# Performance work log

Hardware: AMD Instinct MI355X
Metric: run time of the kernel (lower is better)

The kernel has to match this reference:

```python
import jax, jax.numpy as jnp
import numpy as np

K = 3  # TAGConv default number of hops
N, E = 50000, 800000
F_X, F_POS, HID, OUT = 6, 2, 64, 10


def _tagconv(x, W, b, src, dst, norm, n):
    # TAGConv: out = sum_{k=0}^{K} (A_norm^k x) @ W[k] + b
    out = x @ W[0]
    h = x
    for k in range(1, K + 1):
        # one propagate step: gather from src, weight, scatter-sum to dst
        h = jax.ops.segment_sum(norm[:, None] * h[src], dst, num_segments=n)
        out = out + h @ W[k]
    return out + b


def setup_inputs() -> dict:
    key = jax.random.key(0)
    ks = jax.random.split(key, 12)
    x = jax.random.normal(ks[0], (N, F_X), dtype=jnp.float32)
    pos = jax.random.normal(ks[1], (N, F_POS), dtype=jnp.float32)
    edge_index = jax.random.randint(ks[2], (2, E), 0, N, dtype=jnp.int64)
    edge_attr = jax.random.uniform(ks[3], (E,), dtype=jnp.float32)
    s = 0.1
    W1 = jax.random.normal(ks[4], (K + 1, F_X + F_POS, HID), dtype=jnp.float32) * s
    b1 = jnp.zeros((HID,), dtype=jnp.float32)
    W2 = jax.random.normal(ks[5], (K + 1, HID, HID), dtype=jnp.float32) * s
    b2 = jnp.zeros((HID,), dtype=jnp.float32)
    W3 = jax.random.normal(ks[6], (K + 1, HID, OUT), dtype=jnp.float32) * s
    b3 = jnp.zeros((OUT,), dtype=jnp.float32)
    return {"x": x, "pos": pos, "edge_attr": edge_attr,
            "W1": W1, "b1": b1, "W2": W2, "b2": b2, "W3": W3, "b3": b3,
            "edge_index": edge_index}


def reference(x, pos, edge_attr, W1, b1, W2, b2, W3, b3, edge_index):
    n = x.shape[0]
    src, dst = edge_index[0], edge_index[1]
    # gcn_norm (no self loops, as in TAGConv): deg over destination (col)
    deg = jax.ops.segment_sum(edge_attr, dst, num_segments=n)
    dinv = jnp.where(deg > 0, jax.lax.rsqrt(deg), jnp.zeros_like(deg))
    norm = dinv[src] * edge_attr * dinv[dst]
    h = jnp.concatenate([x, pos], axis=1)
    h = jax.nn.relu(_tagconv(h, W1, b1, src, dst, norm, n))
    # F.dropout with training=False is identity (eval reference)
    h = jax.nn.relu(_tagconv(h, W2, b2, src, dst, norm, n))
    h = _tagconv(h, W3, b3, src, dst, norm, n)
    return jax.nn.log_softmax(h, axis=1)
```

## Files before the change

kernel.cpp:

```cpp
#include <hip/hip_runtime.h>
#include <math.h>


#define NN 50000
#define EE 800000
#define HID 64
#define NOUT 10
#define CH 512

#define NB 391
#define CAP 2400
#define K1_EPB 4096

typedef __attribute__((ext_vector_type(8))) short bf16x8;
typedef __attribute__((ext_vector_type(4))) float f32x4;

__device__ __forceinline__ unsigned bf16rnd(float x) {
    unsigned u = __float_as_uint(x);
    return (u + 0x7FFFu + ((u >> 16) & 1u)) >> 16;
}
__device__ __forceinline__ unsigned packbf2(float a, float b) {
    return bf16rnd(a) | (bf16rnd(b) << 16);
}
__device__ __forceinline__ float bflo(unsigned u) { return __uint_as_float(u << 16); }
__device__ __forceinline__ float bfhi(unsigned u) { return __uint_as_float(u & 0xFFFF0000u); }

__global__ __launch_bounds__(512) void bucket_scatter_kernel(
        const int* __restrict__ src, const int* __restrict__ dst,
        const float* __restrict__ ea, int* __restrict__ cursor,
        int2* __restrict__ regions, int e) {
    __shared__ int hist[NB];
    __shared__ int base[NB];
    int tid = threadIdx.x;
    int e0 = blockIdx.x * K1_EPB;
    int e1 = e0 + K1_EPB; if (e1 > e) e1 = e;
    for (int i = tid; i < NB; i += 512) hist[i] = 0;
    __syncthreads();
    for (int i = e0 + tid; i < e1; i += 512)
        atomicAdd(&hist[dst[i] >> 7], 1);
    __syncthreads();
    for (int b = tid; b < NB; b += 512) {
        int c = hist[b];
        base[b] = (c > 0) ? atomicAdd(&cursor[b], c) : 0;
        hist[b] = 0;
    }
    __syncthreads();
    for (int i = e0 + tid; i < e1; i += 512) {
        int d = dst[i];
        int b = d >> 7;
        int r = atomicAdd(&hist[b], 1);
        int pos = base[b] + r;
        if (pos < CAP)
            regions[(size_t)b * CAP + pos] =
                make_int2(((d & 127) << 16) | src[i], __float_as_int(ea[i]));
    }
}

__global__ __launch_bounds__(512) void bucket_build_kernel(
        const int* __restrict__ cursor, int2* __restrict__ regions,
        float* __restrict__ dinv, int* __restrict__ row_start, int n) {
    __shared__ int2 rec[CAP];
    __shared__ int hist[128];
    __shared__ float easum[128];
    __shared__ float dl[128];
    __shared__ int off[129];
    __shared__ int lcur[128];
    int b = blockIdx.x;
    int tid = threadIdx.x;
    int cnt = cursor[b]; if (cnt > CAP) cnt = CAP;
    size_t rb = (size_t)b * CAP;
    if (tid < 128) { hist[tid] = 0; easum[tid] = 0.f; lcur[tid] = 0; }
    __syncthreads();
    for (int i = tid; i < cnt; i += 512) {
        int2 r = regions[rb + i];
        rec[i] = r;
        int f = r.x >> 16;
        atomicAdd(&hist[f], 1);
        atomicAdd(&easum[f], __int_as_float(r.y));
    }
    __syncthreads();
    if (tid < 128) {
        int lane = tid & 63;
        int v = hist[tid];
        for (int o2 = 1; o2 < 64; o2 <<= 1) {
            int y = __shfl_up(v, o2, 64);
            if (lane >= o2) v += y;
        }
        off[tid + 1] = v;
        float s2 = easum[tid];
        dl[tid] = (s2 > 0.f) ? rsqrtf(s2) : 0.f;
    }
    __syncthreads();
    if (tid == 255) off[0] = 0;
    if (tid >= 64 && tid < 128) off[tid + 1] += off[64];
    __syncthreads();
    if (tid < 128) {
        int node = b * 128 + tid;
        if (node <= n) row_start[node] = b * CAP + off[tid];
        if (node < n)  dinv[node] = dl[tid];
    }
    __syncthreads();
    for (int i = tid; i < cnt; i += 512) {
        int2 r = rec[i];
        int f = r.x >> 16;
        int s = r.x & 0xFFFF;
        int p = atomicAdd(&lcur[f], 1);
        float w0 = __int_as_float(r.y) * dl[f];
        regions[rb + off[f] + p] = make_int2(s, __float_as_int(w0));
    }
}

__global__ __launch_bounds__(256) void srcscale_kernel(
        const int* __restrict__ cursor, const float* __restrict__ dinv,
        int2* __restrict__ regions) {
    int i = blockIdx.x * blockDim.x + threadIdx.x;
    int b = i / CAP;
    if (b >= NB) return;
    int off = i - b * CAP;
    int cnt = cursor[b]; if (cnt > CAP) cnt = CAP;
    if (off >= cnt) return;
    int2 r = regions[i];
    r.y = __float_as_int(__int_as_float(r.y) * dinv[r.x]);
    regions[i] = r;
}

__global__ __launch_bounds__(256) void pack1_kernel(const float* __restrict__ x,
                                                    const float* __restrict__ pos,
                                                    unsigned short* __restrict__ B1, int n) {
    int i = blockIdx.x * blockDim.x + threadIdx.x;
    if (i >= n) return;
    float2 a = *reinterpret_cast<const float2*>(x + (size_t)i * 6);
    float2 b = *reinterpret_cast<const float2*>(x + (size_t)i * 6 + 2);
    float2 c = *reinterpret_cast<const float2*>(x + (size_t)i * 6 + 4);
    float2 p = *reinterpret_cast<const float2*>(pos + (size_t)i * 2);
    uint4 o;
    o.x = packbf2(a.x, a.y);
    o.y = packbf2(b.x, b.y);
    o.z = packbf2(c.x, c.y);
    o.w = packbf2(p.x, p.y);
    *reinterpret_cast<uint4*>(B1 + (size_t)i * 32) = o;
}

__global__ __launch_bounds__(256) void prop8b_kernel(const int* __restrict__ row_start,
                                                     const int* __restrict__ cursor,
                                                     const int2* __restrict__ edges,
                                                     const unsigned short* __restrict__ Gin,
                                                     unsigned short* __restrict__ Gout, int n) {
    constexpr int TEAM = 8, NPB = 32;
    __shared__ int2 se[CH];
    int tid = threadIdx.x;
    int nb = blockIdx.x * NPB;
    int node = nb + tid / TEAM;
    int es = tid % TEAM;
    int nbEnd = (nb + NPB < n) ? (nb + NPB) : n;
    int bkt = nb >> 7;
    int cc = cursor[bkt]; if (cc > CAP) cc = CAP;
    int ce = bkt * CAP + cc;
    int blkBeg = row_start[nb];
    int blkEnd = row_start[nbEnd]; if (blkEnd > ce) blkEnd = ce;
    int beg = 0, end = 0;
    if (node < n) {
        beg = row_start[node];
        end = row_start[node + 1]; if (end > ce) end = ce;
    }
    float a0 = 0.f, a1 = 0.f, a2 = 0.f, a3 = 0.f, a4 = 0.f, a5 = 0.f, a6 = 0.f, a7 = 0.f;
    for (int base = blkBeg; base < blkEnd; base += CH) {
        int m = blkEnd - base; if (m > CH) m = CH;
        __syncthreads();
        for (int i = tid; i < m; i += 256) se[i] = edges[base + i];
        __syncthreads();
        int lo = (beg > base) ? (beg - base) : 0;
        int hi = ((end < base + m) ? end : (base + m)) - base;
        for (int i = lo + es; i < hi; i += TEAM) {
            int2 e = se[i];
            float w = __int_as_float(e.y);
            const uint4 v = *reinterpret_cast<const uint4*>(Gin + (size_t)e.x * 32);
            a0 += w * bflo(v.x); a1 += w * bfhi(v.x);
            a2 += w * bflo(v.y); a3 += w * bfhi(v.y);
            a4 += w * bflo(v.z); a5 += w * bfhi(v.z);
            a6 += w * bflo(v.w); a7 += w * bfhi(v.w);
        }
    }
    #pragma unroll
    for (int msk = 1; msk < TEAM; msk <<= 1) {
        a0 += __shfl_xor(a0, msk); a1 += __shfl_xor(a1, msk);
        a2 += __shfl_xor(a2, msk); a3 += __shfl_xor(a3, msk);
        a4 += __shfl_xor(a4, msk); a5 += __shfl_xor(a5, msk);
        a6 += __shfl_xor(a6, msk); a7 += __shfl_xor(a7, msk);
    }
    if (node < n && es == 0) {
        uint4 o;
        o.x = packbf2(a0, a1);
        o.y = packbf2(a2, a3);
        o.z = packbf2(a4, a5);
        o.w = packbf2(a6, a7);
        *reinterpret_cast<uint4*>(Gout + (size_t)node * 32) = o;
    }
}

template <int TPN, int ES, bool ACC>
__global__ __launch_bounds__(256) void prop_kernel(const int* __restrict__ row_start,
                                                   const int* __restrict__ cursor,
                                                   const int2* __restrict__ edges,
                                                   const float* __restrict__ hin, int in_stride,
                                                   float* __restrict__ hout, int out_stride, int n) {
    constexpr int TEAM = TPN * ES;
    constexpr int NPB = 256 / TEAM;
    __shared__ int2 se[CH];
    int tid = threadIdx.x;
    int nb = blockIdx.x * NPB;
    int node = nb + tid / TEAM;
    int t = tid % TEAM;
    int es = t / TPN;
    int lane = t % TPN;
    int nbEnd = (nb + NPB < n) ? (nb + NPB) : n;
    int bkt = nb >> 7;
    int cc = cursor[bkt]; if (cc > CAP) cc = CAP;
    int ce = bkt * CAP + cc;
    int blkBeg = row_start[nb];
    int blkEnd = row_start[nbEnd]; if (blkEnd > ce) blkEnd = ce;
    int beg = 0, end = 0;
    if (node < n) {
        beg = row_start[node];
        end = row_start[node + 1]; if (end > ce) end = ce;
    }
    float ax = 0.f, ay = 0.f, az = 0.f, aw = 0.f;
    for (int base = blkBeg; base < blkEnd; base += CH) {
        int m = blkEnd - base; if (m > CH) m = CH;
        __syncthreads();
        for (int i = tid; i < m; i += 256) se[i] = edges[base + i];
        __syncthreads();
        int lo = (beg > base) ? (beg - base) : 0;
        int hi = ((end < base + m) ? end : (base + m)) - base;
        for (int i = lo + es; i < hi; i += ES) {
            int2 e = se[i];
            float w = __int_as_float(e.y);
            const float4 v = *reinterpret_cast<const float4*>(hin + (size_t)e.x * in_stride + lane * 4);
            ax += w * v.x; ay += w * v.y; az += w * v.z; aw += w * v.w;
        }
    }
    #pragma unroll
    for (int msk = TPN; msk < TEAM; msk <<= 1) {
        ax += __shfl_xor(ax, msk);
        ay += __shfl_xor(ay, msk);
        az += __shfl_xor(az, msk);
        aw += __shfl_xor(aw, msk);
    }
    if (node < n && es == 0) {
        float4* po = reinterpret_cast<float4*>(hout + (size_t)node * out_stride + lane * 4);
        float4 r = make_float4(ax, ay, az, aw);
        if (ACC) { float4 o = *po; r.x += o.x; r.y += o.y; r.z += o.z; r.w += o.w; }
        *po = r;
    }
}

__global__ __launch_bounds__(256) void prop64b_kernel(const int* __restrict__ row_start,
                                                      const int* __restrict__ cursor,
                                                      const int2* __restrict__ edges,
                                                      const unsigned short* __restrict__ Gin,
                                                      unsigned short* __restrict__ Gout, int n) {
    constexpr int TPN = 8, ES = 4, TEAM = 32, NPB = 8;
    __shared__ int2 se[CH];
    int tid = threadIdx.x;
    int nb = blockIdx.x * NPB;
    int node = nb + tid / TEAM;
    int t = tid % TEAM;
    int es = t / TPN;
    int lane = t % TPN;
    int nbEnd = (nb + NPB < n) ? (nb + NPB) : n;
    int bkt = nb >> 7;
    int cc = cursor[bkt]; if (cc > CAP) cc = CAP;
    int ce = bkt * CAP + cc;
    int blkBeg = row_start[nb];
    int blkEnd = row_start[nbEnd]; if (blkEnd > ce) blkEnd = ce;
    int beg = 0, end = 0;
    if (node < n) {
        beg = row_start[node];
        end = row_start[node + 1]; if (end > ce) end = ce;
    }
    float a0 = 0.f, a1 = 0.f, a2 = 0.f, a3 = 0.f, a4 = 0.f, a5 = 0.f, a6 = 0.f, a7 = 0.f;
    for (int base = blkBeg; base < blkEnd; base += CH) {
        int m = blkEnd - base; if (m > CH) m = CH;
        __syncthreads();
        for (int i = tid; i < m; i += 256) se[i] = edges[base + i];
        __syncthreads();
        int lo = (beg > base) ? (beg - base) : 0;
        int hi = ((end < base + m) ? end : (base + m)) - base;
        for (int i = lo + es; i < hi; i += ES) {
            int2 e = se[i];
            float w = __int_as_float(e.y);
            const uint4 v = *reinterpret_cast<const uint4*>(Gin + (size_t)e.x * 256 + lane * 8);
            a0 += w * bflo(v.x); a1 += w * bfhi(v.x);
            a2 += w * bflo(v.y); a3 += w * bfhi(v.y);
            a4 += w * bflo(v.z); a5 += w * bfhi(v.z);
            a6 += w * bflo(v.w); a7 += w * bfhi(v.w);
        }
    }
    #pragma unroll
    for (int msk = TPN; msk < TEAM; msk <<= 1) {
        a0 += __shfl_xor(a0, msk); a1 += __shfl_xor(a1, msk);
        a2 += __shfl_xor(a2, msk); a3 += __shfl_xor(a3, msk);
        a4 += __shfl_xor(a4, msk); a5 += __shfl_xor(a5, msk);
        a6 += __shfl_xor(a6, msk); a7 += __shfl_xor(a7, msk);
    }
    if (node < n && es == 0) {
        uint4 o;
        o.x = packbf2(a0, a1);
        o.y = packbf2(a2, a3);
        o.z = packbf2(a4, a5);
        o.w = packbf2(a6, a7);
        *reinterpret_cast<uint4*>(Gout + (size_t)node * 256 + lane * 8) = o;
    }
}

__global__ __launch_bounds__(256) void prop_final_kernel(const int* __restrict__ row_start,
                                                         const int* __restrict__ cursor,
                                                         const int2* __restrict__ edges,
                                                         const float* __restrict__ hin,
                                                         const float* __restrict__ g0,
                                                         const float* __restrict__ b3,
                                                         float* __restrict__ out, int n) {
    constexpr int TPN = 4, ES = 2, TEAM = 8, NPB = 32;
    __shared__ int2 se[CH];
    int tid = threadIdx.x;
    int nb = blockIdx.x * NPB;
    int node = nb + tid / TEAM;
    int t = tid % TEAM;
    int es = t / TPN;
    int lane = t % TPN;
    int nbEnd = (nb + NPB < n) ? (nb + NPB) : n;
    int bkt = nb >> 7;
    int cc = cursor[bkt]; if (cc > CAP) cc = CAP;
    int ce = bkt * CAP + cc;
    int blkBeg = row_start[nb];
    int blkEnd = row_start[nbEnd]; if (blkEnd > ce) blkEnd = ce;
    int beg = 0, end = 0;
    if (node < n) {
        beg = row_start[node];
        end = row_start[node + 1]; if (end > ce) end = ce;
    }
    float ax = 0.f, ay = 0.f, az = 0.f, aw = 0.f;
    for (int base = blkBeg; base < blkEnd; base += CH) {
        int m = blkEnd - base; if (m > CH) m = CH;
        __syncthreads();
        for (int i = tid; i < m; i += 256) se[i] = edges[base + i];
        __syncthreads();
        int lo = (beg > base) ? (beg - base) : 0;
        int hi = ((end < base + m) ? end : (base + m)) - base;
        for (int i = lo + es; i < hi; i += ES) {
            int2 e = se[i];
            float w = __int_as_float(e.y);
            const float4 v = *reinterpret_cast<const float4*>(hin + (size_t)e.x * 64 + lane * 4);
            ax += w * v.x; ay += w * v.y; az += w * v.z; aw += w * v.w;
        }
    }
    ax += __shfl_xor(ax, TPN);
    ay += __shfl_xor(ay, TPN);
    az += __shfl_xor(az, TPN);
    aw += __shfl_xor(aw, TPN);
    if (node < n && es == 0) {
        const float4 g = *reinterpret_cast<const float4*>(g0 + (size_t)node * 64 + lane * 4);
        float vv[4] = {ax + g.x, ay + g.y, az + g.z, aw + g.w};
        int c0 = lane * 4;
        float mloc = -1e30f;
        #pragma unroll
        for (int c = 0; c < 4; ++c) {
            int col = c0 + c;
            if (col < NOUT) { vv[c] += b3[col]; mloc = fmaxf(mloc, vv[c]); }
        }
        float mo = fmaxf(mloc, __shfl_xor(mloc, 1));
        mo = fmaxf(mo, __shfl_xor(mo, 2));
        float sl = 0.f;
        #pragma unroll
        for (int c = 0; c < 4; ++c) {
            int col = c0 + c;
            if (col < NOUT) sl += __expf(vv[c] - mo);
        }
        sl += __shfl_xor(sl, 1);
        sl += __shfl_xor(sl, 2);
        float ls = __logf(sl);
        #pragma unroll
        for (int c = 0; c < 4; ++c) {
            int col = c0 + c;
            if (col < NOUT) out[(size_t)node * NOUT + col] = vv[c] - mo - ls;
        }
    }
}

template <int FIN, int KC, int EPI, int WMODE, int INBF16, int OUTBF16>
__global__ __launch_bounds__(256) void mm2_kernel(const void* __restrict__ hraw, int hstride,
                                                  const float* __restrict__ W,
                                                  const float* __restrict__ bias,
                                                  void* __restrict__ outraw, int ostride, int n) {
    constexpr int HP = 68;
    __shared__ float HsT[KC * HP];
    __shared__ float Ws[KC * 64];
    int tid = threadIdx.x;
    int ndq = tid >> 4;
    int f4  = tid & 15;
    int nd  = tid & 63;
    int wv  = tid >> 6;
    int nodeBase = blockIdx.x * 64;

    float4 acc0 = make_float4(0.f, 0.f, 0.f, 0.f);
    float4 acc1 = make_float4(0.f, 0.f, 0.f, 0.f);
    float4 acc2 = make_float4(0.f, 0.f, 0.f, 0.f);
    float4 acc3 = make_float4(0.f, 0.f, 0.f, 0.f);

    for (int kc = 0; kc < FIN; kc += KC) {
        if (WMODE == 0) {
            for (int i = tid * 4; i < KC * 64; i += 1024)
                *reinterpret_cast<float4*>(&Ws[i]) =
                    *reinterpret_cast<const float4*>(&W[(size_t)kc * 64 + i]);
        } else {
            for (int i = tid; i < KC * 64; i += 256) {
                int r = i >> 6, c = i & 63;
                int k = c >> 4, j = c & 15;
                Ws[i] = (j < NOUT) ? W[((size_t)k * FIN + kc + r) * NOUT + j] : 0.f;
            }
        }
        int node = nodeBase + nd;
        if constexpr (INBF16) {
            const unsigned short* hb = (const unsigned short*)hraw;
            constexpr int KPT = KC / 4;
            int k0 = wv * KPT;
            #pragma unroll
            for (int q = 0; q < KPT / 8; ++q) {
                uint4 v = make_uint4(0, 0, 0, 0);
                if (node < n)
                    v = *reinterpret_cast<const uint4*>(hb + (size_t)node * hstride + kc + k0 + q * 8);
                int kk = k0 + q * 8;
                HsT[(kk + 0) * HP + nd] = bflo(v.x); HsT[(kk + 1) * HP + nd] = bfhi(v.x);
                HsT[(kk + 2) * HP + nd] = bflo(v.y); HsT[(kk + 3) * HP + nd] = bfhi(v.y);
                HsT[(kk + 4) * HP + nd] = bflo(v.z); HsT[(kk + 5) * HP + nd] = bfhi(v.z);
                HsT[(kk + 6) * HP + nd] = bflo(v.w); HsT[(kk + 7) * HP + nd] = bfhi(v.w);
            }
        } else {
            const float* hf = (const float*)hraw;
            #pragma unroll
            for (int r = 0; r < KC / 16; ++r) {
                int k0 = wv * 4 + r * 16;
                float4 hv = make_float4(0.f, 0.f, 0.f, 0.f);
                if (node < n)
                    hv = *reinterpret_cast<const float4*>(&hf[(size_t)node * hstride + kc + k0]);
                HsT[(k0 + 0) * HP + nd] = hv.x;
                HsT[(k0 + 1) * HP + nd] = hv.y;
                HsT[(k0 + 2) * HP + nd] = hv.z;
                HsT[(k0 + 3) * HP + nd] = hv.w;
            }
        }
        __syncthreads();
        #pragma unroll 8
        for (int k = 0; k < KC; ++k) {
            const float4 hq = *reinterpret_cast<const float4*>(&HsT[k * HP + ndq * 4]);
            const float4 wq = *reinterpret_cast<const float4*>(&Ws[k * 64 + f4 * 4]);
            acc0.x += hq.x * wq.x; acc0.y += hq.x * wq.y; acc0.z += hq.x * wq.z; acc0.w += hq.x * wq.w;
            acc1.x += hq.y * wq.x; acc1.y += hq.y * wq.y; acc1.z += hq.y * wq.z; acc1.w += hq.y * wq.w;
            acc2.x += hq.z * wq.x; acc2.y += hq.z * wq.y; acc2.z += hq.z * wq.z; acc2.w += hq.z * wq.w;
            acc3.x += hq.w * wq.x; acc3.y += hq.w * wq.y; acc3.z += hq.w * wq.z; acc3.w += hq.w * wq.w;
        }
        __syncthreads();
    }

    float4 bv = make_float4(0.f, 0.f, 0.f, 0.f);
    if (EPI == 1) bv = *reinterpret_cast<const float4*>(&bias[f4 * 4]);
    float4 accs[4] = {acc0, acc1, acc2, acc3};
    #pragma unroll
    for (int i = 0; i < 4; ++i) {
        int node = nodeBase + ndq * 4 + i;
        if (node < n) {
            float4 a = accs[i];
            if (EPI == 1) {
                a.x = fmaxf(a.x + bv.x, 0.f); a.y = fmaxf(a.y + bv.y, 0.f);
                a.z = fmaxf(a.z + bv.z, 0.f); a.w = fmaxf(a.w + bv.w, 0.f);
            }
            if constexpr (OUTBF16) {
                unsigned short* ob = (unsigned short*)outraw;
                uint2 o;
                o.x = packbf2(a.x, a.y);
                o.y = packbf2(a.z, a.w);
                *reinterpret_cast<uint2*>(ob + (size_t)node * ostride + f4 * 4) = o;
            } else {
                float* of = (float*)outraw;
                *reinterpret_cast<float4*>(of + (size_t)node * ostride + f4 * 4) = a;
            }
        }
    }
}

__global__ __launch_bounds__(256) void mm23_kernel(const unsigned short* __restrict__ G,
                                                   const float* __restrict__ W2,
                                                   const float* __restrict__ b2,
                                                   const float* __restrict__ W3,
                                                   float* __restrict__ T, int n) {
    constexpr int HP = 68;
    __shared__ __align__(16) char smem[33792];
    unsigned short* w2s = (unsigned short*)smem;
    float* HsT = (float*)smem;
    float* Ws  = (float*)(smem + 64 * HP * 4);
    int tid = threadIdx.x;
    int wave = tid >> 6;
    int lane = tid & 63;
    int nodeBase = blockIdx.x * 64;

    for (int slot = tid; slot < 2048; slot += 256) {
        int l = slot & 63;
        int s = (slot >> 6) & 7;
        int t = slot >> 9;
        int k0 = s * 32 + ((l >> 4) << 3);
        int col = t * 16 + (l & 15);
        unsigned short tmp[8];
        #pragma unroll
        for (int j = 0; j < 8; ++j)
            tmp[j] = (unsigned short)bf16rnd(W2[(size_t)(k0 + j) * 64 + col]);
        *reinterpret_cast<uint4*>(w2s + slot * 8) = *reinterpret_cast<const uint4*>(tmp);
    }
    __syncthreads();

    int arow = nodeBase + wave * 16 + (lane & 15);
    bool aval = (arow < n);
    const unsigned short* arp = G + (size_t)arow * 256 + ((lane >> 4) << 3);
    f32x4 acc0 = {0.f, 0.f, 0.f, 0.f}, acc1 = {0.f, 0.f, 0.f, 0.f};
    f32x4 acc2 = {0.f, 0.f, 0.f, 0.f}, acc3 = {0.f, 0.f, 0.f, 0.f};
    #pragma unroll
    for (int s = 0; s < 8; ++s) {
        bf16x8 a = {};
        if (aval) a = *reinterpret_cast<const bf16x8*>(arp + s * 32);
        const unsigned short* wb = w2s + ((size_t)s * 64 + lane) * 8;
        bf16x8 bf0 = *reinterpret_cast<const bf16x8*>(wb);
        bf16x8 bf1 = *reinterpret_cast<const bf16x8*>(wb + 4096);
        bf16x8 bf2 = *reinterpret_cast<const bf16x8*>(wb + 8192);
        bf16x8 bf3 = *reinterpret_cast<const bf16x8*>(wb + 12288);
        acc0 = __builtin_amdgcn_mfma_f32_16x16x32_bf16(a, bf0, acc0, 0, 0, 0);
        acc1 = __builtin_amdgcn_mfma_f32_16x16x32_bf16(a, bf1, acc1, 0, 0, 0);
        acc2 = __builtin_amdgcn_mfma_f32_16x16x32_bf16(a, bf2, acc2, 0, 0, 0);
        acc3 = __builtin_amdgcn_mfma_f32_16x16x32_bf16(a, bf3, acc3, 0, 0, 0);
    }
    __syncthreads();

    {
        int c = lane & 15;
        int rbase = wave * 16 + (lane >> 4) * 4;
        f32x4 accs[4] = {acc0, acc1, acc2, acc3};
        #pragma unroll
        for (int t = 0; t < 4; ++t) {
            int col = t * 16 + c;
            float bb = b2[col];
            #pragma unroll
            for (int r = 0; r < 4; ++r) {
                float v = accs[t][r] + bb;
                HsT[col * HP + rbase + r] = v > 0.f ? v : 0.f;
            }
        }
    }
    for (int i = tid; i < 64 * 64; i += 256) {
        int r = i >> 6, c2 = i & 63;
        int k = c2 >> 4, j = c2 & 15;
        Ws[i] = (j < NOUT) ? W3[((size_t)k * 64 + r) * NOUT + j] : 0.f;
    }
    __syncthreads();

    int ndq = tid >> 4;
    int f4  = tid & 15;
    float4 t0 = make_float4(0.f, 0.f, 0.f, 0.f);
    float4 t1 = make_float4(0.f, 0.f, 0.f, 0.f);
    float4 t2 = make_float4(0.f, 0.f, 0.f, 0.f);
    float4 t3 = make_float4(0.f, 0.f, 0.f, 0.f);
    #pragma unroll 8
    for (int k = 0; k < 64; ++k) {
        const float4 hq = *reinterpret_cast<const float4*>(&HsT[k * HP + ndq * 4]);
        const float4 wq = *reinterpret_cast<const float4*>(&Ws[k * 64 + f4 * 4]);
        t0.x += hq.x * wq.x; t0.y += hq.x * wq.y; t0.z += hq.x * wq.z; t0.w += hq.x * wq.w;
        t1.x += hq.y * wq.x; t1.y += hq.y * wq.y; t1.z += hq.y * wq.z; t1.w += hq.y * wq.w;
        t2.x += hq.z * wq.x; t2.y += hq.z * wq.y; t2.z += hq.z * wq.z; t2.w += hq.z * wq.w;
        t3.x += hq.w * wq.x; t3.y += hq.w * wq.y; t3.z += hq.w * wq.z; t3.w += hq.w * wq.w;
    }
    float4 ts[4] = {t0, t1, t2, t3};
    #pragma unroll
    for (int i = 0; i < 4; ++i) {
        int node = nodeBase + ndq * 4 + i;
        if (node < n)
            *reinterpret_cast<float4*>(T + (size_t)node * 64 + f4 * 4) = ts[i];
    }
}

extern "C" void kernel_launch(void* const* d_in, const int* in_sizes, int n_in,
                              void* d_out, int out_size, void* d_ws, size_t ws_size,
                              hipStream_t stream) {
    const float* x   = (const float*)d_in[0];
    const float* pos = (const float*)d_in[1];
    const float* ea  = (const float*)d_in[2];
    const float* W1  = (const float*)d_in[3];
    const float* b1  = (const float*)d_in[4];
    const float* W2  = (const float*)d_in[5];
    const float* b2  = (const float*)d_in[6];
    const float* W3  = (const float*)d_in[7];
    const float* b3  = (const float*)d_in[8];
    const int* eidx  = (const int*)d_in[9];
    const int* src = eidx;
    const int* dst = eidx + EE;
    float* outp = (float*)d_out;

    size_t off = 0;
    char* base = (char*)d_ws;
    auto alloc = [&](size_t bytes) -> void* {
        void* p = base + off;
        off += (bytes + 255) & ~(size_t)255;
        return p;
    };
    int*   cursor    = (int*)alloc(NB * 4);
    int*   row_start = (int*)alloc((NN + 1) * 4);
    float* dinv      = (float*)alloc(NN * 4);
    int2*  edges     = (int2*)alloc((size_t)NB * CAP * 8);
    unsigned short* G  = (unsigned short*)alloc((size_t)NN * 256 * 2);
    unsigned short* B1 = (unsigned short*)alloc((size_t)NN * 32 * 2);
    float* T         = (float*)alloc((size_t)NN * 64 * 4);
    (void)ws_size;

    const int B = 256;
    const int gN = (NN + B - 1) / B;
    const int gK1 = (EE + K1_EPB - 1) / K1_EPB;
    const int gK3 = (NB * CAP + B - 1) / B;
    const int gMM2 = (NN + 63) / 64;
    const int gP32 = (NN + 31) / 32;
    const int gP8  = (NN + 7) / 8;

    hipMemsetAsync(cursor, 0, NB * 4, stream);

    bucket_scatter_kernel<<<gK1, 512, 0, stream>>>(src, dst, ea, cursor, edges, EE);
    bucket_build_kernel<<<NB, 512, 0, stream>>>(cursor, edges, dinv, row_start, NN);
    srcscale_kernel<<<gK3, B, 0, stream>>>(cursor, dinv, edges);

    pack1_kernel<<<gN, B, 0, stream>>>(x, pos, B1, NN);
    prop8b_kernel<<<gP32, B, 0, stream>>>(row_start, cursor, edges, B1,      B1 + 8,  NN);
    prop8b_kernel<<<gP32, B, 0, stream>>>(row_start, cursor, edges, B1 + 8,  B1 + 16, NN);
    prop8b_kernel<<<gP32, B, 0, stream>>>(row_start, cursor, edges, B1 + 16, B1 + 24, NN);
    mm2_kernel<32, 32, 1, 0, 1, 1><<<gMM2, B, 0, stream>>>(B1, 32, W1, b1, G, 256, NN);

    prop64b_kernel<<<gP8, B, 0, stream>>>(row_start, cursor, edges, G,       G + 64,  NN);
    prop64b_kernel<<<gP8, B, 0, stream>>>(row_start, cursor, edges, G + 64,  G + 128, NN);
    prop64b_kernel<<<gP8, B, 0, stream>>>(row_start, cursor, edges, G + 128, G + 192, NN);
    mm23_kernel<<<gMM2, B, 0, stream>>>(G, W2, b2, W3, T, NN);

    prop_kernel<4, 2, true><<<gP32, B, 0, stream>>>(row_start, cursor, edges, T + 48, 64, T + 32, 64, NN);
    prop_kernel<4, 2, true><<<gP32, B, 0, stream>>>(row_start, cursor, edges, T + 32, 64, T + 16, 64, NN);
    prop_final_kernel<<<gP32, B, 0, stream>>>(row_start, cursor, edges, T + 16, T, b3, outp, NN);
}
```

Baseline: 279.4 us.

## Fuse source-degree scaling into first propagation and use MFMA for layer-1 matmul

```diff
diff --git a/kernel.cpp b/kernel.cpp
--- a/kernel.cpp
+++ b/kernel.cpp
@@ -10,7 +10,7 @@
 
 #define NB 391
 #define CAP 2400
-#define K1_EPB 4096
+#define K1_EPB 2048
 
 typedef __attribute__((ext_vector_type(8))) short bf16x8;
 typedef __attribute__((ext_vector_type(4))) float f32x4;
@@ -30,29 +30,35 @@
         const float* __restrict__ ea, int* __restrict__ cursor,
         int2* __restrict__ regions, int e) {
     __shared__ int hist[NB];
-    __shared__ int base[NB];
+    __shared__ int base_s[NB];
     int tid = threadIdx.x;
     int e0 = blockIdx.x * K1_EPB;
     int e1 = e0 + K1_EPB; if (e1 > e) e1 = e;
+    int d[4], s[4];
+    float w[4];
+    int cnt = 0;
+    for (int i = e0 + tid; i < e1; i += 512) {
+        d[cnt] = dst[i]; s[cnt] = src[i]; w[cnt] = ea[i];
+        ++cnt;
+    }
     for (int i = tid; i < NB; i += 512) hist[i] = 0;
     __syncthreads();
-    for (int i = e0 + tid; i < e1; i += 512)
-        atomicAdd(&hist[dst[i] >> 7], 1);
+    for (int j = 0; j < cnt; ++j)
+        atomicAdd(&hist[d[j] >> 7], 1);
     __syncthreads();
     for (int b = tid; b < NB; b += 512) {
         int c = hist[b];
-        base[b] = (c > 0) ? atomicAdd(&cursor[b], c) : 0;
+        base_s[b] = (c > 0) ? atomicAdd(&cursor[b], c) : 0;
         hist[b] = 0;
     }
     __syncthreads();
-    for (int i = e0 + tid; i < e1; i += 512) {
-        int d = dst[i];
-        int b = d >> 7;
+    for (int j = 0; j < cnt; ++j) {
+        int b = d[j] >> 7;
         int r = atomicAdd(&hist[b], 1);
-        int pos = base[b] + r;
+        int pos = base_s[b] + r;
         if (pos < CAP)
             regions[(size_t)b * CAP + pos] =
-                make_int2(((d & 127) << 16) | src[i], __float_as_int(ea[i]));
+                make_int2(((d[j] & 127) << 16) | s[j], __float_as_int(w[j]));
     }
 }
 
@@ -108,20 +114,6 @@
         float w0 = __int_as_float(r.y) * dl[f];
         regions[rb + off[f] + p] = make_int2(s, __float_as_int(w0));
     }
-}
-
-__global__ __launch_bounds__(256) void srcscale_kernel(
-        const int* __restrict__ cursor, const float* __restrict__ dinv,
-        int2* __restrict__ regions) {
-    int i = blockIdx.x * blockDim.x + threadIdx.x;
-    int b = i / CAP;
-    if (b >= NB) return;
-    int off = i - b * CAP;
-    int cnt = cursor[b]; if (cnt > CAP) cnt = CAP;
-    if (off >= cnt) return;
-    int2 r = regions[i];
-    r.y = __float_as_int(__int_as_float(r.y) * dinv[r.x]);
-    regions[i] = r;
 }
 
 __global__ __launch_bounds__(256) void pack1_kernel(const float* __restrict__ x,
@@ -141,9 +133,11 @@
     *reinterpret_cast<uint4*>(B1 + (size_t)i * 32) = o;
 }
 
+template <int SCALE>
 __global__ __launch_bounds__(256) void prop8b_kernel(const int* __restrict__ row_start,
                                                      const int* __restrict__ cursor,
-                                                     const int2* __restrict__ edges,
+                                                     int2* __restrict__ edges,
+                                                     const float* __restrict__ dinv,
                                                      const unsigned short* __restrict__ Gin,
                                                      unsigned short* __restrict__ Gout, int n) {
     constexpr int TEAM = 8, NPB = 32;
@@ -167,7 +161,14 @@
     for (int base = blkBeg; base < blkEnd; base += CH) {
         int m = blkEnd - base; if (m > CH) m = CH;
         __syncthreads();
-        for (int i = tid; i < m; i += 256) se[i] = edges[base + i];
+        for (int i = tid; i < m; i += 256) {
+            int2 r = edges[base + i];
+            if (SCALE) {
+                r.y = __float_as_int(__int_as_float(r.y) * dinv[r.x]);
+                edges[base + i] = r;
+            }
+            se[i] = r;
+        }
         __syncthreads();
         int lo = (beg > base) ? (beg - base) : 0;
         int hi = ((end < base + m) ? end : (base + m)) - base;
@@ -387,104 +388,64 @@
     }
 }
 
-template <int FIN, int KC, int EPI, int WMODE, int INBF16, int OUTBF16>
-__global__ __launch_bounds__(256) void mm2_kernel(const void* __restrict__ hraw, int hstride,
-                                                  const float* __restrict__ W,
-                                                  const float* __restrict__ bias,
-                                                  void* __restrict__ outraw, int ostride, int n) {
-    constexpr int HP = 68;
-    __shared__ float HsT[KC * HP];
-    __shared__ float Ws[KC * 64];
-    int tid = threadIdx.x;
-    int ndq = tid >> 4;
-    int f4  = tid & 15;
-    int nd  = tid & 63;
-    int wv  = tid >> 6;
+__global__ __launch_bounds__(256) void mm1_kernel(const unsigned short* __restrict__ B1,
+                                                  const float* __restrict__ W1,
+                                                  const float* __restrict__ b1,
+                                                  unsigned short* __restrict__ G, int n) {
+    __shared__ unsigned short w1s[2048];
+    __shared__ unsigned short hs[64 * 64];
+    int tid = threadIdx.x;
+    int wave = tid >> 6;
+    int lane = tid & 63;
     int nodeBase = blockIdx.x * 64;
 
-    float4 acc0 = make_float4(0.f, 0.f, 0.f, 0.f);
-    float4 acc1 = make_float4(0.f, 0.f, 0.f, 0.f);
-    float4 acc2 = make_float4(0.f, 0.f, 0.f, 0.f);
-    float4 acc3 = make_float4(0.f, 0.f, 0.f, 0.f);
-
-    for (int kc = 0; kc < FIN; kc += KC) {
-        if (WMODE == 0) {
-            for (int i = tid * 4; i < KC * 64; i += 1024)
-                *reinterpret_cast<float4*>(&Ws[i]) =
-                    *reinterpret_cast<const float4*>(&W[(size_t)kc * 64 + i]);
-        } else {
-            for (int i = tid; i < KC * 64; i += 256) {
-                int r = i >> 6, c = i & 63;
-                int k = c >> 4, j = c & 15;
-                Ws[i] = (j < NOUT) ? W[((size_t)k * FIN + kc + r) * NOUT + j] : 0.f;
+    {
+        int l = tid & 63;
+        int t = tid >> 6;
+        int k0 = (l >> 4) << 3;
+        int col = t * 16 + (l & 15);
+        unsigned short tmp[8];
+        #pragma unroll
+        for (int j = 0; j < 8; ++j)
+            tmp[j] = (unsigned short)bf16rnd(W1[(size_t)(k0 + j) * 64 + col]);
+        *reinterpret_cast<uint4*>(w1s + tid * 8) = *reinterpret_cast<const uint4*>(tmp);
+    }
+    __syncthreads();
+
+    int arow = nodeBase + wave * 16 + (lane & 15);
+    bf16x8 a = {};
+    if (arow < n)
+        a = *reinterpret_cast<const bf16x8*>(B1 + (size_t)arow * 32 + ((lane >> 4) << 3));
+    const unsigned short* wb = w1s + lane * 8;
+    f32x4 acc0 = {0.f, 0.f, 0.f, 0.f}, acc1 = {0.f, 0.f, 0.f, 0.f};
+    f32x4 acc2 = {0.f, 0.f, 0.f, 0.f}, acc3 = {0.f, 0.f, 0.f, 0.f};
+    acc0 = __builtin_amdgcn_mfma_f32_16x16x32_bf16(a, *reinterpret_cast<const bf16x8*>(wb),        acc0, 0, 0, 0);
+    acc1 = __builtin_amdgcn_mfma_f32_16x16x32_bf16(a, *reinterpret_cast<const bf16x8*>(wb + 512),  acc1, 0, 0, 0);
+    acc2 = __builtin_amdgcn_mfma_f32_16x16x32_bf16(a, *reinterpret_cast<const bf16x8*>(wb + 1024), acc2, 0, 0, 0);
+    acc3 = __builtin_amdgcn_mfma_f32_16x16x32_bf16(a, *reinterpret_cast<const bf16x8*>(wb + 1536), acc3, 0, 0, 0);
+
+    {
+        int c = lane & 15;
+        int rbase = wave * 16 + (lane >> 4) * 4;
+        f32x4 accs[4] = {acc0, acc1, acc2, acc3};
+        #pragma unroll
+        for (int t = 0; t < 4; ++t) {
+            int col = t * 16 + c;
+            float bb = b1[col];
+            #pragma unroll
+            for (int r = 0; r < 4; ++r) {
+                float v = accs[t][r] + bb;
+                hs[(rbase + r) * 64 + col] = (unsigned short)bf16rnd(v > 0.f ? v : 0.f);
             }
         }
+    }
+    __syncthreads();
+    for (int i = tid; i < 512; i += 256) {
+        int nd = i >> 3, ch = i & 7;
         int node = nodeBase + nd;
-        if constexpr (INBF16) {
-            const unsigned short* hb = (const unsigned short*)hraw;
-            constexpr int KPT = KC / 4;
-            int k0 = wv * KPT;
-            #pragma unroll
-            for (int q = 0; q < KPT / 8; ++q) {
-                uint4 v = make_uint4(0, 0, 0, 0);
-                if (node < n)
-                    v = *reinterpret_cast<const uint4*>(hb + (size_t)node * hstride + kc + k0 + q * 8);
-                int kk = k0 + q * 8;
-                HsT[(kk + 0) * HP + nd] = bflo(v.x); HsT[(kk + 1) * HP + nd] = bfhi(v.x);
-                HsT[(kk + 2) * HP + nd] = bflo(v.y); HsT[(kk + 3) * HP + nd] = bfhi(v.y);
-                HsT[(kk + 4) * HP + nd] = bflo(v.z); HsT[(kk + 5) * HP + nd] = bfhi(v.z);
-                HsT[(kk + 6) * HP + nd] = bflo(v.w); HsT[(kk + 7) * HP + nd] = bfhi(v.w);
-            }
-        } else {
-            const float* hf = (const float*)hraw;
-            #pragma unroll
-            for (int r = 0; r < KC / 16; ++r) {
-                int k0 = wv * 4 + r * 16;
-                float4 hv = make_float4(0.f, 0.f, 0.f, 0.f);
-                if (node < n)
-                    hv = *reinterpret_cast<const float4*>(&hf[(size_t)node * hstride + kc + k0]);
-                HsT[(k0 + 0) * HP + nd] = hv.x;
-                HsT[(k0 + 1) * HP + nd] = hv.y;
-                HsT[(k0 + 2) * HP + nd] = hv.z;
-                HsT[(k0 + 3) * HP + nd] = hv.w;
-            }
-        }
-        __syncthreads();
-        #pragma unroll 8
-        for (int k = 0; k < KC; ++k) {
-            const float4 hq = *reinterpret_cast<const float4*>(&HsT[k * HP + ndq * 4]);
-            const float4 wq = *reinterpret_cast<const float4*>(&Ws[k * 64 + f4 * 4]);
-            acc0.x += hq.x * wq.x; acc0.y += hq.x * wq.y; acc0.z += hq.x * wq.z; acc0.w += hq.x * wq.w;
-            acc1.x += hq.y * wq.x; acc1.y += hq.y * wq.y; acc1.z += hq.y * wq.z; acc1.w += hq.y * wq.w;
-            acc2.x += hq.z * wq.x; acc2.y += hq.z * wq.y; acc2.z += hq.z * wq.z; acc2.w += hq.z * wq.w;
-            acc3.x += hq.w * wq.x; acc3.y += hq.w * wq.y; acc3.z += hq.w * wq.z; acc3.w += hq.w * wq.w;
-        }
-        __syncthreads();
-    }
-
-    float4 bv = make_float4(0.f, 0.f, 0.f, 0.f);
-    if (EPI == 1) bv = *reinterpret_cast<const float4*>(&bias[f4 * 4]);
-    float4 accs[4] = {acc0, acc1, acc2, acc3};
-    #pragma unroll
-    for (int i = 0; i < 4; ++i) {
-        int node = nodeBase + ndq * 4 + i;
-        if (node < n) {
-            float4 a = accs[i];
-            if (EPI == 1) {
-                a.x = fmaxf(a.x + bv.x, 0.f); a.y = fmaxf(a.y + bv.y, 0.f);
-                a.z = fmaxf(a.z + bv.z, 0.f); a.w = fmaxf(a.w + bv.w, 0.f);
-            }
-            if constexpr (OUTBF16) {
-                unsigned short* ob = (unsigned short*)outraw;
-                uint2 o;
-                o.x = packbf2(a.x, a.y);
-                o.y = packbf2(a.z, a.w);
-                *reinterpret_cast<uint2*>(ob + (size_t)node * ostride + f4 * 4) = o;
-            } else {
-                float* of = (float*)outraw;
-                *reinterpret_cast<float4*>(of + (size_t)node * ostride + f4 * 4) = a;
-            }
-        }
+        if (node < n)
+            *reinterpret_cast<uint4*>(G + (size_t)node * 256 + ch * 8) =
+                *reinterpret_cast<const uint4*>(hs + nd * 64 + ch * 8);
     }
 }
 
@@ -620,7 +581,6 @@
     const int B = 256;
     const int gN = (NN + B - 1) / B;
     const int gK1 = (EE + K1_EPB - 1) / K1_EPB;
-    const int gK3 = (NB * CAP + B - 1) / B;
     const int gMM2 = (NN + 63) / 64;
     const int gP32 = (NN + 31) / 32;
     const int gP8  = (NN + 7) / 8;
@@ -629,13 +589,12 @@
 
     bucket_scatter_kernel<<<gK1, 512, 0, stream>>>(src, dst, ea, cursor, edges, EE);
     bucket_build_kernel<<<NB, 512, 0, stream>>>(cursor, edges, dinv, row_start, NN);
-    srcscale_kernel<<<gK3, B, 0, stream>>>(cursor, dinv, edges);
 
     pack1_kernel<<<gN, B, 0, stream>>>(x, pos, B1, NN);
-    prop8b_kernel<<<gP32, B, 0, stream>>>(row_start, cursor, edges, B1,      B1 + 8,  NN);
-    prop8b_kernel<<<gP32, B, 0, stream>>>(row_start, cursor, edges, B1 + 8,  B1 + 16, NN);
-    prop8b_kernel<<<gP32, B, 0, stream>>>(row_start, cursor, edges, B1 + 16, B1 + 24, NN);
-    mm2_kernel<32, 32, 1, 0, 1, 1><<<gMM2, B, 0, stream>>>(B1, 32, W1, b1, G, 256, NN);
+    prop8b_kernel<1><<<gP32, B, 0, stream>>>(row_start, cursor, edges, dinv, B1,      B1 + 8,  NN);
+    prop8b_kernel<0><<<gP32, B, 0, stream>>>(row_start, cursor, edges, dinv, B1 + 8,  B1 + 16, NN);
+    prop8b_kernel<0><<<gP32, B, 0, stream>>>(row_start, cursor, edges, dinv, B1 + 16, B1 + 24, NN);
+    mm1_kernel<<<gMM2, B, 0, stream>>>(B1, W1, b1, G, NN);
 
     prop64b_kernel<<<gP8, B, 0, stream>>>(row_start, cursor, edges, G,       G + 64,  NN);
     prop64b_kernel<<<gP8, B, 0, stream>>>(row_start, cursor, edges, G + 64,  G + 128, NN);
```

Result: faster. 273.7 us (-2.1%).
